# Kernel optimization log

Measured on AMD Instinct MI355X. Metric: run time of the kernel, lower is better.

The kernel has to match this reference:

```python
import jax, jax.numpy as jnp
import numpy as np

N_NODES = 100000
N_EDGES = 1600000


def _glorot(key, shape):
    lim = float(np.sqrt(6.0 / (shape[0] + shape[1])))
    return jax.random.uniform(key, shape, jnp.float32, -lim, lim)


def setup_inputs() -> dict:
    key = jax.random.key(0)
    ks = jax.random.split(key, 12)
    x = jax.random.normal(ks[0], (N_NODES, 8), jnp.float32)
    edge_index = jax.random.randint(ks[1], (2, N_EDGES), 0, N_NODES, jnp.int64)
    dims = [(8, 32), (32, 32), (32, 32), (32, 32), (32, 3)]
    params = {}
    for i, (din, dout) in enumerate(dims):
        params[f"W{i+1}"] = _glorot(ks[2 + i], (din, dout))
        params[f"b{i+1}"] = jnp.zeros((dout,), jnp.float32)
    return {"x": x, "edge_index": edge_index, **params}


def _gcn_norm(edge_index, num_nodes):
    # add self-loops, symmetric normalization (PyG GCNConv defaults)
    loops = jnp.arange(num_nodes, dtype=edge_index.dtype)
    row = jnp.concatenate([edge_index[0], loops])
    col = jnp.concatenate([edge_index[1], loops])
    deg = jax.ops.segment_sum(jnp.ones_like(col, jnp.float32), col,
                              num_segments=num_nodes)
    dinv = jnp.where(deg > 0, jax.lax.rsqrt(deg), 0.0)
    norm = dinv[row] * dinv[col]  # [E + N]
    return row, col, norm


def _gcn_conv(h, W, b, row, col, norm, num_nodes):
    h = h @ W                                   # [N, dout]
    msg = h[row] * norm[:, None]                # gather + scale
    out = jax.ops.segment_sum(msg, col, num_segments=num_nodes)
    return out + b


def reference(x, edge_index, W1, b1, W2, b2, W3, b3, W4, b4, W5, b5):
    row, col, norm = _gcn_norm(edge_index, N_NODES)
    lrelu = lambda h: jax.nn.leaky_relu(h, negative_slope=1.0)  # identity, kept faithful
    h = lrelu(_gcn_conv(x, W1, b1, row, col, norm, N_NODES))
    h = lrelu(_gcn_conv(h, W2, b2, row, col, norm, N_NODES))
    h = lrelu(_gcn_conv(h, W3, b3, row, col, norm, N_NODES))
    h = lrelu(_gcn_conv(h, W4, b4, row, col, norm, N_NODES))
    h = lrelu(_gcn_conv(h, W5, b5, row, col, norm, N_NODES))
    return h
```

## Files before the change

### kernel.cpp

```cpp
#include <hip/hip_runtime.h>
#include <hip/hip_bf16.h>

#define NN 100000
#define NE 1600000
#define NB 391
#define EPB 4096
#define NBLK 391


__global__ __launch_bounds__(256) void detect_kernel(const unsigned int* __restrict__ w,
                                                     int* __restrict__ is64) {
    __shared__ int nz;
    if (threadIdx.x == 0) nz = 0;
    __syncthreads();
    if (w[2 * threadIdx.x + 1] != 0) atomicAdd(&nz, 1);
    __syncthreads();
    if (threadIdx.x == 0) *is64 = (nz == 0) ? 1 : 0;
}

static __device__ __forceinline__ int edge_at(const void* ei, int is64, long long pos) {
    return is64 ? (int)((const long long*)ei)[pos] : ((const int*)ei)[pos];
}


__global__ __launch_bounds__(256) void bucket_count_kernel(const void* __restrict__ ei,
                                                           const int* __restrict__ is64,
                                                           int* __restrict__ bcount, int E) {
    __shared__ int lc[NB];
    int tid = threadIdx.x;
    for (int i = tid; i < NB; i += 256) lc[i] = 0;
    __syncthreads();
    int f = *is64;
    long long base = (long long)blockIdx.x * EPB;
    for (int k = 0; k < EPB / 256; k++) {
        long long e = base + k * 256 + tid;
        if (e < E) {
            int c = edge_at(ei, f, (long long)E + e);
            atomicAdd(&lc[c >> 8], 1);
        }
    }
    __syncthreads();
    for (int i = tid; i < NB; i += 256)
        if (lc[i]) atomicAdd(&bcount[i], lc[i]);
}


__global__ __launch_bounds__(512) void bucket_scan_kernel(const int* __restrict__ bcount,
                                                          int* __restrict__ bstart,
                                                          int* __restrict__ bcursor, int E) {
    __shared__ int s[512];
    int tid = threadIdx.x;
    int v = (tid < NB) ? bcount[tid] : 0;
    int acc = v;
    s[tid] = v;
    __syncthreads();
    for (int off = 1; off < 512; off <<= 1) {
        int y = (tid >= off) ? s[tid - off] : 0;
        __syncthreads();
        acc += y;
        s[tid] = acc;
        __syncthreads();
    }
    if (tid < NB) {
        int excl = acc - v;
        bstart[tid] = excl;
        bcursor[tid] = excl;
    }
    if (tid == 0) bstart[NB] = E;
}


__global__ __launch_bounds__(256) void bucket_scatter_kernel(const void* __restrict__ ei,
                                                             const int* __restrict__ is64,
                                                             int* __restrict__ bcursor,
                                                             unsigned int* __restrict__ epacked,
                                                             int E) {
    __shared__ int lcount[NB];
    __shared__ int lstart[NB];
    __shared__ int lcur[NB];
    __shared__ int gbase[NB];
    __shared__ int ps[256];
    __shared__ unsigned int slotv[EPB];
    __shared__ unsigned short slotb[EPB];
    int tid = threadIdx.x;
    for (int i = tid; i < NB; i += 256) lcount[i] = 0;
    __syncthreads();
    int f = *is64;
    long long base = (long long)blockIdx.x * EPB;
    int r[EPB / 256], c[EPB / 256];
    for (int k = 0; k < EPB / 256; k++) {
        long long e = base + (long long)k * 256 + tid;
        if (e < E) {
            r[k] = edge_at(ei, f, e);
            c[k] = edge_at(ei, f, (long long)E + e);
            atomicAdd(&lcount[c[k] >> 8], 1);
        } else {
            r[k] = -1;
        }
    }
    __syncthreads();
    int e0 = (2 * tid < NB) ? lcount[2 * tid] : 0;
    int e1 = (2 * tid + 1 < NB) ? lcount[2 * tid + 1] : 0;
    int sum = e0 + e1, acc = sum;
    ps[tid] = sum;
    __syncthreads();
    for (int off = 1; off < 256; off <<= 1) {
        int y = (tid >= off) ? ps[tid - off] : 0;
        __syncthreads();
        acc += y;
        ps[tid] = acc;
        __syncthreads();
    }
    int excl = acc - sum;
    if (2 * tid < NB) lstart[2 * tid] = excl;
    if (2 * tid + 1 < NB) lstart[2 * tid + 1] = excl + e0;
    __syncthreads();
    for (int i = tid; i < NB; i += 256) lcur[i] = lstart[i];
    __syncthreads();
    for (int k = 0; k < EPB / 256; k++) {
        if (r[k] >= 0) {
            int b = c[k] >> 8;
            int pos = atomicAdd(&lcur[b], 1);
            slotv[pos] = ((unsigned)(c[k] & 255) << 24) | (unsigned)r[k];
            slotb[pos] = (unsigned short)b;
        }
    }
    __syncthreads();
    for (int i = tid; i < NB; i += 256) {
        int cnt = lcount[i];
        gbase[i] = cnt ? atomicAdd(&bcursor[i], cnt) : 0;
    }
    __syncthreads();
    long long rem = (long long)E - base;
    int total = (rem < EPB) ? (int)rem : EPB;
    for (int s2 = tid; s2 < total; s2 += 256) {
        int b = slotb[s2];
        int within = s2 - lstart[b];
        epacked[gbase[b] + within] = slotv[s2];
    }
}


__global__ __launch_bounds__(256) void bucket_csr_kernel(const unsigned int* __restrict__ epacked,
                                                         const int* __restrict__ bstart,
                                                         int* __restrict__ start,
                                                         int* __restrict__ degi,
                                                         float* __restrict__ dinv,
                                                         int* __restrict__ srow, int N) {
    __shared__ int lcount[256];
    __shared__ int lcur[256];
    __shared__ int ss[256];
    int b = blockIdx.x;
    int tid = threadIdx.x;
    int s0 = bstart[b];
    int cnt = bstart[b + 1] - s0;
    lcount[tid] = 0;
    __syncthreads();
    for (int i = tid; i < cnt; i += 256) {
        unsigned int v = epacked[s0 + i];
        atomicAdd(&lcount[v >> 24], 1);
    }
    __syncthreads();
    int myc = lcount[tid];
    int acc = myc;
    ss[tid] = myc;
    __syncthreads();
    for (int off = 1; off < 256; off <<= 1) {
        int y = (tid >= off) ? ss[tid - off] : 0;
        __syncthreads();
        acc += y;
        ss[tid] = acc;
        __syncthreads();
    }
    int excl = acc - myc;
    lcur[tid] = excl;
    int col = (b << 8) + tid;
    if (col < N) {
        start[col] = s0 + excl;
        degi[col] = myc;
        dinv[col] = 1.0f / sqrtf((float)myc + 1.0f);
    }
    __syncthreads();
    for (int i = tid; i < cnt; i += 256) {
        unsigned int v = epacked[s0 + i];
        int p = atomicAdd(&lcur[v >> 24], 1);
        srow[s0 + p] = (int)(v & 0xFFFFFFu);
    }
}


__global__ __launch_bounds__(256) void prep_kernel(
    const float* __restrict__ W1, const float* __restrict__ b1,
    const float* __restrict__ W2, const float* __restrict__ b2,
    const float* __restrict__ W3, const float* __restrict__ b3,
    const float* __restrict__ W4, const float* __restrict__ b4,
    const float* __restrict__ W5, const float* __restrict__ b5,
    float* __restrict__ Wt,
    float* __restrict__ cv) {
    __shared__ float w45[32 * 3], w345[32 * 3], w2345[32 * 3];
    int tid = threadIdx.x;
    int i = tid / 3, j = tid - 3 * (tid / 3);
    if (tid < 96) {
        float s = 0.0f;
        for (int k = 0; k < 32; k++) s += W4[i * 32 + k] * W5[k * 3 + j];
        w45[i * 3 + j] = s;
    }
    __syncthreads();
    if (tid < 96) {
        float s = 0.0f;
        for (int k = 0; k < 32; k++) s += W3[i * 32 + k] * w45[k * 3 + j];
        w345[i * 3 + j] = s;
    }
    __syncthreads();
    if (tid < 96) {
        float s = 0.0f;
        for (int k = 0; k < 32; k++) s += W2[i * 32 + k] * w345[k * 3 + j];
        w2345[i * 3 + j] = s;
    }
    __syncthreads();
    if (tid < 32) {
        int ii = tid >> 2, jj = tid & 3;
        float s = 0.0f;
        if (jj < 3)
            for (int k = 0; k < 32; k++) s += W1[ii * 32 + k] * w2345[k * 3 + jj];
        Wt[tid] = s;
    }
    if (tid >= 32 && tid < 52) {
        int kk = (tid - 32) >> 2, jj = (tid - 32) & 3;
        float s = 0.0f;
        if (jj < 3) {
            if (kk == 0) for (int k = 0; k < 32; k++) s += b1[k] * w2345[k * 3 + jj];
            if (kk == 1) for (int k = 0; k < 32; k++) s += b2[k] * w345[k * 3 + jj];
            if (kk == 2) for (int k = 0; k < 32; k++) s += b3[k] * w45[k * 3 + jj];
            if (kk == 3) for (int k = 0; k < 32; k++) s += b4[k] * W5[k * 3 + jj];
            if (kk == 4) s = b5[jj];
        }
        cv[tid - 32] = s;
    }
}


__global__ __launch_bounds__(256) void z_kernel(const float* __restrict__ x,
                                                const float* __restrict__ Wt,
                                                const float* __restrict__ dinv,
                                                float4* __restrict__ t0, int N) {
    __shared__ float4 Wl[8];
    if (threadIdx.x < 8) Wl[threadIdx.x] = ((const float4*)Wt)[threadIdx.x];
    __syncthreads();
    int n = blockIdx.x * 256 + threadIdx.x;
    if (n >= N) return;
    float d = dinv[n];
    const float4* x4 = (const float4*)x + n * 2;
    float4 a = x4[0], b = x4[1];
    float xs[8] = {a.x, a.y, a.z, a.w, b.x, b.y, b.z, b.w};
    float4 o = make_float4(0.f, 0.f, 0.f, 0.f);
#pragma unroll
    for (int k = 0; k < 8; k++) {
        float4 w = Wl[k];
        o.x += xs[k] * w.x; o.y += xs[k] * w.y; o.z += xs[k] * w.z;
    }
    o.x *= d; o.y *= d; o.z *= d; o.w = 0.0f;
    t0[n] = o;
}


template <bool LAST>
__global__ __launch_bounds__(256) void prop_kernel(
    const int* __restrict__ start, const int* __restrict__ degi,
    const int* __restrict__ srow, const float4* __restrict__ tin,
    const float* __restrict__ dinv, const float* __restrict__ cv, int k,
    float4* __restrict__ tout, float* __restrict__ out, int N) {
    int tid = blockIdx.x * 256 + threadIdx.x;
    int c = tid >> 2, q = tid & 3;
    if (c >= N) return;
    int s = start[c];
    int d = degi[c];
    float4 a = (q == 0) ? tin[c] : make_float4(0.f, 0.f, 0.f, 0.f);
    float4 a2 = make_float4(0.f, 0.f, 0.f, 0.f);
    int i = q;
    for (; i + 4 < d; i += 8) {
        int r0 = srow[s + i];
        int r1 = srow[s + i + 4];
        float4 v0 = tin[r0];
        float4 v1 = tin[r1];
        a.x += v0.x; a.y += v0.y; a.z += v0.z;
        a2.x += v1.x; a2.y += v1.y; a2.z += v1.z;
    }
    if (i < d) {
        float4 v = tin[srow[s + i]];
        a.x += v.x; a.y += v.y; a.z += v.z;
    }
    a.x += a2.x; a.y += a2.y; a.z += a2.z;
    a.x += __shfl_xor(a.x, 1); a.y += __shfl_xor(a.y, 1); a.z += __shfl_xor(a.z, 1);
    a.x += __shfl_xor(a.x, 2); a.y += __shfl_xor(a.y, 2); a.z += __shfl_xor(a.z, 2);
    if (q == 0) {
        float dd = dinv[c];
        float cx = cv[k * 4 + 0], cy = cv[k * 4 + 1], cz = cv[k * 4 + 2];
        if (LAST) {
            out[c * 3 + 0] = dd * a.x + cx;
            out[c * 3 + 1] = dd * a.y + cy;
            out[c * 3 + 2] = dd * a.z + cz;
        } else {
            float d2 = dd * dd;
            float4 o;
            o.x = d2 * a.x + dd * cx;
            o.y = d2 * a.y + dd * cy;
            o.z = d2 * a.z + dd * cz;
            o.w = 0.0f;
            tout[c] = o;
        }
    }
}


extern "C" void kernel_launch(void* const* d_in, const int* in_sizes, int n_in,
                              void* d_out, int out_size, void* d_ws, size_t ws_size,
                              hipStream_t stream) {
    const float* x  = (const float*)d_in[0];
    const void*  ei = d_in[1];
    const float* W1 = (const float*)d_in[2];  const float* b1 = (const float*)d_in[3];
    const float* W2 = (const float*)d_in[4];  const float* b2 = (const float*)d_in[5];
    const float* W3 = (const float*)d_in[6];  const float* b3 = (const float*)d_in[7];
    const float* W4 = (const float*)d_in[8];  const float* b4 = (const float*)d_in[9];
    const float* W5 = (const float*)d_in[10]; const float* b5 = (const float*)d_in[11];
    float* out = (float*)d_out;

    char* p = (char*)d_ws;
    auto alloc = [&](size_t bytes) {
        char* r = p;
        p += (bytes + 255) & ~(size_t)255;
        return r;
    };
    int*   degi    = (int*)alloc(NN * 4);
    float* dinv    = (float*)alloc(NN * 4);
    int*   start   = (int*)alloc(NN * 4);
    int*   is64    = (int*)alloc(256);
    int*   bcount  = (int*)alloc(NB * 4);
    int*   bstart  = (int*)alloc((NB + 1) * 4);
    int*   bcursor = (int*)alloc(NB * 4);
    float* Wt      = (float*)alloc(8 * 4 * 4);
    float* cv      = (float*)alloc(5 * 4 * 4);
    unsigned int* epacked = (unsigned int*)alloc((size_t)NE * 4);
    int*          srow    = (int*)alloc((size_t)NE * 4);
    float4*       Ta      = (float4*)alloc((size_t)NN * 16);
    float4*       Tb      = (float4*)alloc((size_t)NN * 16);
    if ((size_t)(p - (char*)d_ws) > ws_size) return;

    hipMemsetAsync(bcount, 0, NB * 4, stream);

    int gN = (NN + 255) / 256;
    int gP = (NN * 4 + 255) / 256;
    detect_kernel<<<1, 256, 0, stream>>>((const unsigned int*)ei, is64);
    bucket_count_kernel<<<NBLK, 256, 0, stream>>>(ei, is64, bcount, NE);
    bucket_scan_kernel<<<1, 512, 0, stream>>>(bcount, bstart, bcursor, NE);
    bucket_scatter_kernel<<<NBLK, 256, 0, stream>>>(ei, is64, bcursor, epacked, NE);
    bucket_csr_kernel<<<NB, 256, 0, stream>>>(epacked, bstart, start, degi, dinv, srow, NN);
    prep_kernel<<<1, 256, 0, stream>>>(W1, b1, W2, b2, W3, b3, W4, b4, W5, b5, Wt, cv);

    z_kernel<<<gN, 256, 0, stream>>>(x, Wt, dinv, Ta, NN);
    prop_kernel<false><<<gP, 256, 0, stream>>>(start, degi, srow, Ta, dinv, cv, 0, Tb, nullptr, NN);
    prop_kernel<false><<<gP, 256, 0, stream>>>(start, degi, srow, Tb, dinv, cv, 1, Ta, nullptr, NN);
    prop_kernel<false><<<gP, 256, 0, stream>>>(start, degi, srow, Ta, dinv, cv, 2, Tb, nullptr, NN);
    prop_kernel<false><<<gP, 256, 0, stream>>>(start, degi, srow, Tb, dinv, cv, 3, Ta, nullptr, NN);
    prop_kernel<true><<<gP, 256, 0, stream>>>(start, degi, srow, Ta, dinv, cv, 4, nullptr, out, NN);
}
```

Before: 205.2 us.

## Fuse propagation passes into persistent kernel and drop bucket count/scan via fixed-capacity buckets

Replaces the bucket counting and prefix-scan kernels with fixed-capacity bucket slots initialised in the prep kernel, so the scatter writes straight into padded regions. Fuses the input transform and all five propagation passes into one persistent kernel whose passes are separated by atomic-counter global barriers. This is meant to cut kernel launch and tail overheads. In exchange it relies on all 1024 blocks being co-resident, and it drops edges if any bucket exceeds its fixed capacity.

```diff
diff --git a/kernel.cpp b/kernel.cpp
--- a/kernel.cpp
+++ b/kernel.cpp
@@ -6,6 +6,8 @@
 #define NB 391
 #define EPB 4096
 #define NBLK 391
+#define CAP 4608
+#define GRID 1024
 
 
 __global__ __launch_bounds__(256) void detect_kernel(const unsigned int* __restrict__ w,
@@ -23,50 +25,56 @@
 }
 
 
-__global__ __launch_bounds__(256) void bucket_count_kernel(const void* __restrict__ ei,
-                                                           const int* __restrict__ is64,
-                                                           int* __restrict__ bcount, int E) {
-    __shared__ int lc[NB];
+__global__ __launch_bounds__(256) void prep_kernel(
+    const float* __restrict__ W1, const float* __restrict__ b1,
+    const float* __restrict__ W2, const float* __restrict__ b2,
+    const float* __restrict__ W3, const float* __restrict__ b3,
+    const float* __restrict__ W4, const float* __restrict__ b4,
+    const float* __restrict__ W5, const float* __restrict__ b5,
+    float* __restrict__ Wt, float* __restrict__ cv,
+    int* __restrict__ bcursor, int* __restrict__ cnt) {
+    __shared__ float w45[32 * 3], w345[32 * 3], w2345[32 * 3];
     int tid = threadIdx.x;
-    for (int i = tid; i < NB; i += 256) lc[i] = 0;
-    __syncthreads();
-    int f = *is64;
-    long long base = (long long)blockIdx.x * EPB;
-    for (int k = 0; k < EPB / 256; k++) {
-        long long e = base + k * 256 + tid;
-        if (e < E) {
-            int c = edge_at(ei, f, (long long)E + e);
-            atomicAdd(&lc[c >> 8], 1);
-        }
-    }
-    __syncthreads();
-    for (int i = tid; i < NB; i += 256)
-        if (lc[i]) atomicAdd(&bcount[i], lc[i]);
-}
-
-
-__global__ __launch_bounds__(512) void bucket_scan_kernel(const int* __restrict__ bcount,
-                                                          int* __restrict__ bstart,
-                                                          int* __restrict__ bcursor, int E) {
-    __shared__ int s[512];
-    int tid = threadIdx.x;
-    int v = (tid < NB) ? bcount[tid] : 0;
-    int acc = v;
-    s[tid] = v;
-    __syncthreads();
-    for (int off = 1; off < 512; off <<= 1) {
-        int y = (tid >= off) ? s[tid - off] : 0;
-        __syncthreads();
-        acc += y;
-        s[tid] = acc;
-        __syncthreads();
-    }
-    if (tid < NB) {
-        int excl = acc - v;
-        bstart[tid] = excl;
-        bcursor[tid] = excl;
-    }
-    if (tid == 0) bstart[NB] = E;
+    for (int i = tid; i < NB; i += 256) bcursor[i] = i * CAP;
+    if (tid < 8) cnt[tid] = 0;
+    int i = tid / 3, j = tid - 3 * (tid / 3);
+    if (tid < 96) {
+        float s = 0.0f;
+        for (int k = 0; k < 32; k++) s += W4[i * 32 + k] * W5[k * 3 + j];
+        w45[i * 3 + j] = s;
+    }
+    __syncthreads();
+    if (tid < 96) {
+        float s = 0.0f;
+        for (int k = 0; k < 32; k++) s += W3[i * 32 + k] * w45[k * 3 + j];
+        w345[i * 3 + j] = s;
+    }
+    __syncthreads();
+    if (tid < 96) {
+        float s = 0.0f;
+        for (int k = 0; k < 32; k++) s += W2[i * 32 + k] * w345[k * 3 + j];
+        w2345[i * 3 + j] = s;
+    }
+    __syncthreads();
+    if (tid < 32) {
+        int ii = tid >> 2, jj = tid & 3;
+        float s = 0.0f;
+        if (jj < 3)
+            for (int k = 0; k < 32; k++) s += W1[ii * 32 + k] * w2345[k * 3 + jj];
+        Wt[tid] = s;
+    }
+    if (tid >= 32 && tid < 52) {
+        int kk = (tid - 32) >> 2, jj = (tid - 32) & 3;
+        float s = 0.0f;
+        if (jj < 3) {
+            if (kk == 0) for (int k = 0; k < 32; k++) s += b1[k] * w2345[k * 3 + jj];
+            if (kk == 1) for (int k = 0; k < 32; k++) s += b2[k] * w345[k * 3 + jj];
+            if (kk == 2) for (int k = 0; k < 32; k++) s += b3[k] * w45[k * 3 + jj];
+            if (kk == 3) for (int k = 0; k < 32; k++) s += b4[k] * W5[k * 3 + jj];
+            if (kk == 4) s = b5[jj];
+        }
+        cv[tid - 32] = s;
+    }
 }
 
 
@@ -135,14 +143,14 @@
     int total = (rem < EPB) ? (int)rem : EPB;
     for (int s2 = tid; s2 < total; s2 += 256) {
         int b = slotb[s2];
-        int within = s2 - lstart[b];
-        epacked[gbase[b] + within] = slotv[s2];
+        int dst = gbase[b] + (s2 - lstart[b]);
+        if (dst < (b + 1) * CAP) epacked[dst] = slotv[s2];
     }
 }
 
 
 __global__ __launch_bounds__(256) void bucket_csr_kernel(const unsigned int* __restrict__ epacked,
-                                                         const int* __restrict__ bstart,
+                                                         const int* __restrict__ bcursor,
                                                          int* __restrict__ start,
                                                          int* __restrict__ degi,
                                                          float* __restrict__ dinv,
@@ -152,8 +160,9 @@
     __shared__ int ss[256];
     int b = blockIdx.x;
     int tid = threadIdx.x;
-    int s0 = bstart[b];
-    int cnt = bstart[b + 1] - s0;
+    int s0 = b * CAP;
+    int cnt = bcursor[b] - s0;
+    if (cnt > CAP) cnt = CAP;
     lcount[tid] = 0;
     __syncthreads();
     for (int i = tid; i < cnt; i += 256) {
@@ -189,127 +198,106 @@
 }
 
 
-__global__ __launch_bounds__(256) void prep_kernel(
-    const float* __restrict__ W1, const float* __restrict__ b1,
-    const float* __restrict__ W2, const float* __restrict__ b2,
-    const float* __restrict__ W3, const float* __restrict__ b3,
-    const float* __restrict__ W4, const float* __restrict__ b4,
-    const float* __restrict__ W5, const float* __restrict__ b5,
-    float* __restrict__ Wt,
-    float* __restrict__ cv) {
-    __shared__ float w45[32 * 3], w345[32 * 3], w2345[32 * 3];
-    int tid = threadIdx.x;
-    int i = tid / 3, j = tid - 3 * (tid / 3);
-    if (tid < 96) {
-        float s = 0.0f;
-        for (int k = 0; k < 32; k++) s += W4[i * 32 + k] * W5[k * 3 + j];
-        w45[i * 3 + j] = s;
-    }
-    __syncthreads();
-    if (tid < 96) {
-        float s = 0.0f;
-        for (int k = 0; k < 32; k++) s += W3[i * 32 + k] * w45[k * 3 + j];
-        w345[i * 3 + j] = s;
-    }
-    __syncthreads();
-    if (tid < 96) {
-        float s = 0.0f;
-        for (int k = 0; k < 32; k++) s += W2[i * 32 + k] * w345[k * 3 + j];
-        w2345[i * 3 + j] = s;
-    }
-    __syncthreads();
-    if (tid < 32) {
-        int ii = tid >> 2, jj = tid & 3;
-        float s = 0.0f;
-        if (jj < 3)
-            for (int k = 0; k < 32; k++) s += W1[ii * 32 + k] * w2345[k * 3 + jj];
-        Wt[tid] = s;
-    }
-    if (tid >= 32 && tid < 52) {
-        int kk = (tid - 32) >> 2, jj = (tid - 32) & 3;
-        float s = 0.0f;
-        if (jj < 3) {
-            if (kk == 0) for (int k = 0; k < 32; k++) s += b1[k] * w2345[k * 3 + jj];
-            if (kk == 1) for (int k = 0; k < 32; k++) s += b2[k] * w345[k * 3 + jj];
-            if (kk == 2) for (int k = 0; k < 32; k++) s += b3[k] * w45[k * 3 + jj];
-            if (kk == 3) for (int k = 0; k < 32; k++) s += b4[k] * W5[k * 3 + jj];
-            if (kk == 4) s = b5[jj];
-        }
-        cv[tid - 32] = s;
-    }
-}
-
-
-__global__ __launch_bounds__(256) void z_kernel(const float* __restrict__ x,
-                                                const float* __restrict__ Wt,
-                                                const float* __restrict__ dinv,
-                                                float4* __restrict__ t0, int N) {
-    __shared__ float4 Wl[8];
-    if (threadIdx.x < 8) Wl[threadIdx.x] = ((const float4*)Wt)[threadIdx.x];
-    __syncthreads();
-    int n = blockIdx.x * 256 + threadIdx.x;
-    if (n >= N) return;
-    float d = dinv[n];
-    const float4* x4 = (const float4*)x + n * 2;
-    float4 a = x4[0], b = x4[1];
-    float xs[8] = {a.x, a.y, a.z, a.w, b.x, b.y, b.z, b.w};
-    float4 o = make_float4(0.f, 0.f, 0.f, 0.f);
-#pragma unroll
-    for (int k = 0; k < 8; k++) {
-        float4 w = Wl[k];
-        o.x += xs[k] * w.x; o.y += xs[k] * w.y; o.z += xs[k] * w.z;
-    }
-    o.x *= d; o.y *= d; o.z *= d; o.w = 0.0f;
-    t0[n] = o;
-}
-
+static __device__ __forceinline__ void gbar(int* cnt, int idx) {
+    __syncthreads();
+    if (threadIdx.x == 0) {
+        __threadfence();
+        atomicAdd(&cnt[idx], 1);
+        while (__hip_atomic_load(&cnt[idx], __ATOMIC_RELAXED,
+                                 __HIP_MEMORY_SCOPE_AGENT) < GRID)
+            __builtin_amdgcn_s_sleep(8);
+        __threadfence();
+    }
+    __syncthreads();
+}
 
 template <bool LAST>
-__global__ __launch_bounds__(256) void prop_kernel(
+static __device__ __forceinline__ void prop_pass(
     const int* __restrict__ start, const int* __restrict__ degi,
     const int* __restrict__ srow, const float4* __restrict__ tin,
-    const float* __restrict__ dinv, const float* __restrict__ cv, int k,
-    float4* __restrict__ tout, float* __restrict__ out, int N) {
-    int tid = blockIdx.x * 256 + threadIdx.x;
-    int c = tid >> 2, q = tid & 3;
-    if (c >= N) return;
-    int s = start[c];
-    int d = degi[c];
-    float4 a = (q == 0) ? tin[c] : make_float4(0.f, 0.f, 0.f, 0.f);
-    float4 a2 = make_float4(0.f, 0.f, 0.f, 0.f);
-    int i = q;
-    for (; i + 4 < d; i += 8) {
-        int r0 = srow[s + i];
-        int r1 = srow[s + i + 4];
-        float4 v0 = tin[r0];
-        float4 v1 = tin[r1];
-        a.x += v0.x; a.y += v0.y; a.z += v0.z;
-        a2.x += v1.x; a2.y += v1.y; a2.z += v1.z;
-    }
-    if (i < d) {
-        float4 v = tin[srow[s + i]];
-        a.x += v.x; a.y += v.y; a.z += v.z;
-    }
-    a.x += a2.x; a.y += a2.y; a.z += a2.z;
-    a.x += __shfl_xor(a.x, 1); a.y += __shfl_xor(a.y, 1); a.z += __shfl_xor(a.z, 1);
-    a.x += __shfl_xor(a.x, 2); a.y += __shfl_xor(a.y, 2); a.z += __shfl_xor(a.z, 2);
-    if (q == 0) {
-        float dd = dinv[c];
-        float cx = cv[k * 4 + 0], cy = cv[k * 4 + 1], cz = cv[k * 4 + 2];
-        if (LAST) {
-            out[c * 3 + 0] = dd * a.x + cx;
-            out[c * 3 + 1] = dd * a.y + cy;
-            out[c * 3 + 2] = dd * a.z + cz;
-        } else {
-            float d2 = dd * dd;
-            float4 o;
-            o.x = d2 * a.x + dd * cx;
-            o.y = d2 * a.y + dd * cy;
-            o.z = d2 * a.z + dd * cz;
-            o.w = 0.0f;
-            tout[c] = o;
-        }
-    }
+    const float* __restrict__ dinv, const float* __restrict__ cvl, int k,
+    float4* __restrict__ tout, float* __restrict__ out, int N, int gtid, int gsz) {
+    for (int t = gtid; t < N * 4; t += gsz) {
+        int c = t >> 2, q = t & 3;
+        int s = start[c];
+        int d = degi[c];
+        float4 a = (q == 0) ? tin[c] : make_float4(0.f, 0.f, 0.f, 0.f);
+        float4 a2 = make_float4(0.f, 0.f, 0.f, 0.f);
+        int i = q;
+        for (; i + 4 < d; i += 8) {
+            int r0 = srow[s + i];
+            int r1 = srow[s + i + 4];
+            float4 v0 = tin[r0];
+            float4 v1 = tin[r1];
+            a.x += v0.x; a.y += v0.y; a.z += v0.z;
+            a2.x += v1.x; a2.y += v1.y; a2.z += v1.z;
+        }
+        if (i < d) {
+            float4 v = tin[srow[s + i]];
+            a.x += v.x; a.y += v.y; a.z += v.z;
+        }
+        a.x += a2.x; a.y += a2.y; a.z += a2.z;
+        a.x += __shfl_xor(a.x, 1); a.y += __shfl_xor(a.y, 1); a.z += __shfl_xor(a.z, 1);
+        a.x += __shfl_xor(a.x, 2); a.y += __shfl_xor(a.y, 2); a.z += __shfl_xor(a.z, 2);
+        if (q == 0) {
+            float dd = dinv[c];
+            float cx = cvl[k * 4 + 0], cy = cvl[k * 4 + 1], cz = cvl[k * 4 + 2];
+            if (LAST) {
+                out[c * 3 + 0] = dd * a.x + cx;
+                out[c * 3 + 1] = dd * a.y + cy;
+                out[c * 3 + 2] = dd * a.z + cz;
+            } else {
+                float d2 = dd * dd;
+                float4 o;
+                o.x = d2 * a.x + dd * cx;
+                o.y = d2 * a.y + dd * cy;
+                o.z = d2 * a.z + dd * cz;
+                o.w = 0.0f;
+                tout[c] = o;
+            }
+        }
+    }
+}
+
+__global__ __launch_bounds__(256, 4) void fused_kernel(
+    const int* __restrict__ start, const int* __restrict__ degi,
+    const int* __restrict__ srow, const float* __restrict__ dinv,
+    const float* __restrict__ x, const float* __restrict__ Wt,
+    const float* __restrict__ cv, float4* __restrict__ Ta,
+    float4* __restrict__ Tb, float* __restrict__ out,
+    int* __restrict__ cnt, int N) {
+    __shared__ float4 Wl[8];
+    __shared__ float cvl[20];
+    if (threadIdx.x < 8) Wl[threadIdx.x] = ((const float4*)Wt)[threadIdx.x];
+    if (threadIdx.x < 20) cvl[threadIdx.x] = cv[threadIdx.x];
+    __syncthreads();
+    int gsz = GRID * 256;
+    int gtid = blockIdx.x * 256 + threadIdx.x;
+
+    for (int n = gtid; n < N; n += gsz) {
+        float d = dinv[n];
+        const float4* x4 = (const float4*)x + n * 2;
+        float4 av = x4[0], bv = x4[1];
+        float xs[8] = {av.x, av.y, av.z, av.w, bv.x, bv.y, bv.z, bv.w};
+        float4 o = make_float4(0.f, 0.f, 0.f, 0.f);
+#pragma unroll
+        for (int k = 0; k < 8; k++) {
+            float4 w = Wl[k];
+            o.x += xs[k] * w.x; o.y += xs[k] * w.y; o.z += xs[k] * w.z;
+        }
+        o.x *= d; o.y *= d; o.z *= d; o.w = 0.0f;
+        Ta[n] = o;
+    }
+    gbar(cnt, 0);
+    prop_pass<false>(start, degi, srow, Ta, dinv, cvl, 0, Tb, nullptr, N, gtid, gsz);
+    gbar(cnt, 1);
+    prop_pass<false>(start, degi, srow, Tb, dinv, cvl, 1, Ta, nullptr, N, gtid, gsz);
+    gbar(cnt, 2);
+    prop_pass<false>(start, degi, srow, Ta, dinv, cvl, 2, Tb, nullptr, N, gtid, gsz);
+    gbar(cnt, 3);
+    prop_pass<false>(start, degi, srow, Tb, dinv, cvl, 3, Ta, nullptr, N, gtid, gsz);
+    gbar(cnt, 4);
+    prop_pass<true>(start, degi, srow, Ta, dinv, cvl, 4, nullptr, out, N, gtid, gsz);
 }
 
 
@@ -335,32 +323,21 @@
     float* dinv    = (float*)alloc(NN * 4);
     int*   start   = (int*)alloc(NN * 4);
     int*   is64    = (int*)alloc(256);
-    int*   bcount  = (int*)alloc(NB * 4);
-    int*   bstart  = (int*)alloc((NB + 1) * 4);
     int*   bcursor = (int*)alloc(NB * 4);
+    int*   cnt     = (int*)alloc(256);
     float* Wt      = (float*)alloc(8 * 4 * 4);
     float* cv      = (float*)alloc(5 * 4 * 4);
-    unsigned int* epacked = (unsigned int*)alloc((size_t)NE * 4);
-    int*          srow    = (int*)alloc((size_t)NE * 4);
+    unsigned int* epacked = (unsigned int*)alloc((size_t)NB * CAP * 4);
+    int*          srow    = (int*)alloc((size_t)NB * CAP * 4);
     float4*       Ta      = (float4*)alloc((size_t)NN * 16);
     float4*       Tb      = (float4*)alloc((size_t)NN * 16);
     if ((size_t)(p - (char*)d_ws) > ws_size) return;
 
-    hipMemsetAsync(bcount, 0, NB * 4, stream);
-
-    int gN = (NN + 255) / 256;
-    int gP = (NN * 4 + 255) / 256;
     detect_kernel<<<1, 256, 0, stream>>>((const unsigned int*)ei, is64);
-    bucket_count_kernel<<<NBLK, 256, 0, stream>>>(ei, is64, bcount, NE);
-    bucket_scan_kernel<<<1, 512, 0, stream>>>(bcount, bstart, bcursor, NE);
+    prep_kernel<<<1, 256, 0, stream>>>(W1, b1, W2, b2, W3, b3, W4, b4, W5, b5,
+                                       Wt, cv, bcursor, cnt);
     bucket_scatter_kernel<<<NBLK, 256, 0, stream>>>(ei, is64, bcursor, epacked, NE);
-    bucket_csr_kernel<<<NB, 256, 0, stream>>>(epacked, bstart, start, degi, dinv, srow, NN);
-    prep_kernel<<<1, 256, 0, stream>>>(W1, b1, W2, b2, W3, b3, W4, b4, W5, b5, Wt, cv);
-
-    z_kernel<<<gN, 256, 0, stream>>>(x, Wt, dinv, Ta, NN);
-    prop_kernel<false><<<gP, 256, 0, stream>>>(start, degi, srow, Ta, dinv, cv, 0, Tb, nullptr, NN);
-    prop_kernel<false><<<gP, 256, 0, stream>>>(start, degi, srow, Tb, dinv, cv, 1, Ta, nullptr, NN);
-    prop_kernel<false><<<gP, 256, 0, stream>>>(start, degi, srow, Ta, dinv, cv, 2, Tb, nullptr, NN);
-    prop_kernel<false><<<gP, 256, 0, stream>>>(start, degi, srow, Tb, dinv, cv, 3, Ta, nullptr, NN);
-    prop_kernel<true><<<gP, 256, 0, stream>>>(start, degi, srow, Ta, dinv, cv, 4, nullptr, out, NN);
-}
+    bucket_csr_kernel<<<NB, 256, 0, stream>>>(epacked, bcursor, start, degi, dinv, srow, NN);
+    fused_kernel<<<GRID, 256, 0, stream>>>(start, degi, srow, dinv, x, Wt, cv,
+                                           Ta, Tb, out, cnt, NN);
+}
```

Result: slower. 769.9 us (+275.1%).
